# Kernel optimization log

Measured on AMD Instinct MI355X. Metric: run time of the kernel, lower is better.

The kernel has to match this reference:

```python
import jax, jax.numpy as jnp
import numpy as np
import math

D = 8192      # data_dim = num simplices
B = 8         # batch
E = 131072    # Laplacian nnz (avg degree 16)
HID = 256     # hidden_dim
TDIM = 128    # time_embed_dim


def setup_inputs() -> dict:
    key = jax.random.key(0)
    ks = jax.random.split(key, 16)

    def lin(k, i, o):
        return jax.random.normal(k, (i, o), jnp.float32) / np.sqrt(i).astype(np.float32)

    return {
        "x": jax.random.normal(ks[0], (B, D), jnp.float32),
        "t": jax.random.uniform(ks[1], (B,), jnp.float32),
        "ld_idx": jax.random.randint(ks[2], (2, E), 0, D),
        "ld_val": jax.random.normal(ks[3], (E,), jnp.float32) * 0.1,
        "lu_idx": jax.random.randint(ks[4], (2, E), 0, D),
        "lu_val": jax.random.normal(ks[5], (E,), jnp.float32) * 0.1,
        "W1": jax.random.normal(ks[6], (1, HID, 3), jnp.float32),        # SNN layer1 weight [in, out, 1+down+up]
        "W2": jax.random.normal(ks[7], (HID, 1, 3), jnp.float32) / np.sqrt(HID).astype(np.float32),
        "t_w1": lin(ks[8], TDIM, HID), "t_b1": jnp.zeros((HID,), jnp.float32),
        "t_w2": lin(ks[9], HID, HID), "t_b2": jnp.zeros((HID,), jnp.float32),
        "map_w": lin(ks[10], D, HID), "map_b": jnp.zeros((HID,), jnp.float32),
        "o_w1": lin(ks[11], HID, HID), "o_b1": jnp.zeros((HID,), jnp.float32),
        "o_w2": lin(ks[12], HID, D), "o_b2": jnp.zeros((D,), jnp.float32),
    }


def timestep_embedding(t, dim, max_period=10000):
    half = dim // 2  # dim=128 is even, no zero padding column
    freqs = jnp.exp(-math.log(max_period) * jnp.arange(half, dtype=t.dtype) / half)
    args = t[:, None] * freqs[None, :]
    return jnp.concatenate([jnp.cos(args), jnp.sin(args)], axis=-1)


def spmm(idx, val, x):
    # sparse [N,N] @ dense [N,C] via COO gather + segment-sum scatter
    return jax.ops.segment_sum(val[:, None] * x[idx[1]], idx[0], num_segments=x.shape[0])


def snn_layer(x, W, ld_idx, ld_val, lu_idx, lu_val):
    # conv_order_down = conv_order_up = 1 -> terms: [identity, L_down x, L_up x]
    terms = jnp.stack([x, spmm(ld_idx, ld_val, x), spmm(lu_idx, lu_val, x)], axis=2)  # [N, Cin, 3]
    return jnp.einsum('nik,iok->no', terms, W)


def reference(x, t, ld_idx, ld_val, lu_idx, lu_val, W1, W2,
              t_w1, t_b1, t_w2, t_b2, map_w, map_b, o_w1, o_b1, o_w2, o_b2):
    # time embedding MLP
    t_emb = timestep_embedding(t, TDIM)                    # [B, TDIM]
    t_out = jax.nn.silu(t_emb @ t_w1 + t_b1) @ t_w2 + t_b2  # [B, HID]

    # SNN (2 layers): layer1 update_func=None -> raw y; layer2 update_func='id' -> raw y
    def snn(xi):  # xi: [N]
        h = snn_layer(xi[:, None], W1, ld_idx, ld_val, lu_idx, lu_val)  # [N, HID]
        y = snn_layer(h, W2, ld_idx, ld_val, lu_idx, lu_val)            # [N, 1]
        return y[:, 0]

    x_out = jax.vmap(snn)(x)                               # [B, N]

    # ResNet_FC with 0 res blocks -> just the map Linear
    h = x_out @ map_w + map_b                              # [B, HID]

    out = jax.nn.silu((h + t_out) @ o_w1 + o_b1) @ o_w2 + o_b2  # [B, D]
    return out
```

## Files before the change

kernel.cpp:

```cpp
#include <hip/hip_runtime.h>
#include <math.h>

#define D 8192
#define B 8
#define E 131072
#define HID 256
#define TDIM 128

#define OFF_XT 0
#define OFF_DD 65536
#define OFF_UU 131072
#define OFF_Y  196608
#define OFF_G  262144
#define OFF_SC 264192

__global__ __launch_bounds__(1024) void k_front(
        const float* __restrict__ x, const float* __restrict__ t,
        const float* __restrict__ W1, const float* __restrict__ W2,
        const float* __restrict__ t_w1, const float* __restrict__ t_b1,
        const float* __restrict__ t_w2, const float* __restrict__ t_b2,
        const float* __restrict__ map_b, float* __restrict__ ws)
{
    const int blk = blockIdx.x, tid = threadIdx.x;
    if (blk < 64) {
        int idx = blk * 1024 + tid;
        ws[OFF_XT + idx] = x[(idx & 7) * D + (idx >> 3)];
        ws[OFF_DD + idx] = 0.f;
        ws[OFF_UU + idx] = 0.f;
        ws[OFF_Y  + idx] = 0.f;
        return;
    }
    if (blk < 72) {
        const int b = blk - 64;
        __shared__ float emb[TDIM];
        __shared__ float h1[HID];
        __shared__ float part[4][HID];
        float tb = t[b];
        if (tid < TDIM) {
            int j = tid & 63;
            float freq = expf(-0.14391156831212787f * (float)j);
            float a = tb * freq;
            emb[tid] = (tid < 64) ? cosf(a) : sinf(a);
        }
        __syncthreads();
        const int j = tid & 255, ic = tid >> 8;
        float z = 0.f;
        #pragma unroll 8
        for (int i = ic * 32; i < ic * 32 + 32; i++) z += emb[i] * t_w1[i * HID + j];
        part[ic][j] = z;
        __syncthreads();
        if (tid < HID) {
            float zz = t_b1[tid] + part[0][tid] + part[1][tid] + part[2][tid] + part[3][tid];
            h1[tid] = zz / (1.f + expf(-zz));
        }
        __syncthreads();
        float z2 = 0.f;
        #pragma unroll 8
        for (int i = ic * 64; i < ic * 64 + 64; i++) z2 += h1[i] * t_w2[i * HID + j];
        part[ic][j] = z2;
        __syncthreads();
        if (tid < HID) {
            float zz = t_b2[tid] + part[0][tid] + part[1][tid] + part[2][tid] + part[3][tid];
            (ws + OFF_G)[b * HID + tid] = map_b[tid] + zz;
        }
        return;
    }
    {
        int w = tid >> 6, lane = tid & 63;
        if (w < 9) {
            int jj = w / 3, k = w % 3;
            float acc = 0.f;
            #pragma unroll
            for (int q = 0; q < 4; q++) {
                int i = lane + 64 * q;
                acc += W1[i * 3 + k] * W2[i * 3 + jj];
            }
            #pragma unroll
            for (int off = 32; off > 0; off >>= 1) acc += __shfl_down(acc, off, 64);
            if (lane == 0) (ws + OFF_SC)[jj * 3 + k] = acc;
        }
    }
}

__global__ void k_scat1(const int* __restrict__ ldi, const float* __restrict__ ldv,
                        const int* __restrict__ lui, const float* __restrict__ luv,
                        float* __restrict__ ws)
{
    int gtid = blockIdx.x * 256 + threadIdx.x;
    int b = gtid & 7;
    int e = gtid >> 3;
    const int* idx; const float* val; float* dst;
    if (e < E) { idx = ldi; val = ldv; dst = ws + OFF_DD; }
    else       { e -= E; idx = lui; val = luv; dst = ws + OFF_UU; }
    int row = idx[e];
    int col = idx[E + e];
    float v = val[e];
    atomicAdd(&dst[row * 8 + b], v * ws[OFF_XT + col * 8 + b]);
}

__global__ void k_scat2(const int* __restrict__ ldi, const float* __restrict__ ldv,
                        const int* __restrict__ lui, const float* __restrict__ luv,
                        float* __restrict__ ws)
{
    int gtid = blockIdx.x * 256 + threadIdx.x;
    int b = gtid & 7;
    int e = gtid >> 3;
    const float* sc = ws + OFF_SC;
    const int* idx; const float* val; float c0, c1, c2;
    if (e < E) { idx = ldi; val = ldv; c0 = sc[3]; c1 = sc[4]; c2 = sc[5]; }
    else       { e -= E; idx = lui; val = luv; c0 = sc[6]; c1 = sc[7]; c2 = sc[8]; }
    int row = idx[e];
    int col = idx[E + e];
    float v = val[e];
    int ci = col * 8 + b;
    float h = c0 * ws[OFF_XT + ci] + c1 * ws[OFF_DD + ci] + c2 * ws[OFF_UU + ci];
    atomicAdd(&ws[OFF_Y + row * 8 + b], v * h);
}

__global__ void k_map(const float* __restrict__ map_w, float* __restrict__ ws)
{
    __shared__ float yf[32 * 8];
    int blk = blockIdx.x, tid = threadIdx.x;
    const float* sc = ws + OFF_SC;
    float* g = ws + OFF_G;
    int base = blk * 256;
    yf[tid] = sc[0] * ws[OFF_XT + base + tid] + sc[1] * ws[OFF_DD + base + tid]
            + sc[2] * ws[OFF_UU + base + tid] + ws[OFF_Y + base + tid];
    __syncthreads();
    float acc[8] = {0.f, 0.f, 0.f, 0.f, 0.f, 0.f, 0.f, 0.f};
    int nbase = blk * 32;
    #pragma unroll 4
    for (int r = 0; r < 32; r++) {
        float w = map_w[(nbase + r) * HID + tid];
        #pragma unroll
        for (int b = 0; b < 8; b++) acc[b] += yf[r * 8 + b] * w;
    }
    #pragma unroll
    for (int b = 0; b < 8; b++) atomicAdd(&g[b * HID + tid], acc[b]);
}

__global__ __launch_bounds__(1024) void k_mlpout(
        const float* __restrict__ o_w1, const float* __restrict__ o_b1,
        const float* __restrict__ o_w2, const float* __restrict__ o_b2,
        const float* __restrict__ ws, float* __restrict__ out)
{
    __shared__ float gs[B * HID];
    __shared__ float part[4][B * HID];
    __shared__ float ssl[B * HID];
    const int blk = blockIdx.x, tid = threadIdx.x;
    gs[tid] = ws[OFF_G + tid];
    gs[1024 + tid] = ws[OFF_G + 1024 + tid];
    __syncthreads();
    {
        int j = tid & 255, ic = tid >> 8;
        float z[8] = {0.f, 0.f, 0.f, 0.f, 0.f, 0.f, 0.f, 0.f};
        #pragma unroll 4
        for (int i = ic * 64; i < ic * 64 + 64; i++) {
            float w = o_w1[i * HID + j];
            #pragma unroll
            for (int b = 0; b < 8; b++) z[b] += gs[b * HID + i] * w;
        }
        #pragma unroll
        for (int b = 0; b < 8; b++) part[ic][b * HID + j] = z[b];
    }
    __syncthreads();
    #pragma unroll
    for (int it = 0; it < 2; it++) {
        int P = it * 1024 + tid;
        float zz = o_b1[P & 255] + part[0][P] + part[1][P] + part[2][P] + part[3][P];
        ssl[P] = zz / (1.f + expf(-zz));
    }
    __syncthreads();
    {
        int nl = tid & 255, ic = tid >> 8;
        int n = blk * 256 + nl;
        float acc[8] = {0.f, 0.f, 0.f, 0.f, 0.f, 0.f, 0.f, 0.f};
        #pragma unroll 4
        for (int j = ic * 64; j < ic * 64 + 64; j++) {
            float w = o_w2[j * D + n];
            #pragma unroll
            for (int b = 0; b < 8; b++) acc[b] += ssl[b * HID + j] * w;
        }
        #pragma unroll
        for (int b = 0; b < 8; b++) part[ic][b * HID + nl] = acc[b];
    }
    __syncthreads();
    #pragma unroll
    for (int it = 0; it < 2; it++) {
        int P = it * 1024 + tid;
        int b = P >> 8, nl = P & 255;
        int n = blk * 256 + nl;
        out[b * D + n] = o_b2[n] + part[0][P] + part[1][P] + part[2][P] + part[3][P];
    }
}

extern "C" void kernel_launch(void* const* d_in, const int* in_sizes, int n_in,
                              void* d_out, int out_size, void* d_ws, size_t ws_size,
                              hipStream_t stream)
{
    const float* x     = (const float*)d_in[0];
    const float* t     = (const float*)d_in[1];
    const int*   ldi   = (const int*)  d_in[2];
    const float* ldv   = (const float*)d_in[3];
    const int*   lui   = (const int*)  d_in[4];
    const float* luv   = (const float*)d_in[5];
    const float* W1    = (const float*)d_in[6];
    const float* W2    = (const float*)d_in[7];
    const float* t_w1  = (const float*)d_in[8];
    const float* t_b1  = (const float*)d_in[9];
    const float* t_w2  = (const float*)d_in[10];
    const float* t_b2  = (const float*)d_in[11];
    const float* map_w = (const float*)d_in[12];
    const float* map_b = (const float*)d_in[13];
    const float* o_w1  = (const float*)d_in[14];
    const float* o_b1  = (const float*)d_in[15];
    const float* o_w2  = (const float*)d_in[16];
    const float* o_b2  = (const float*)d_in[17];
    float* out = (float*)d_out;
    float* ws  = (float*)d_ws;

    k_front<<<73, 1024, 0, stream>>>(x, t, W1, W2, t_w1, t_b1, t_w2, t_b2, map_b, ws);
    k_scat1<<<2 * E * 8 / 256, 256, 0, stream>>>(ldi, ldv, lui, luv, ws);
    k_scat2<<<2 * E * 8 / 256, 256, 0, stream>>>(ldi, ldv, lui, luv, ws);
    k_map<<<256, 256, 0, stream>>>(map_w, ws);
    k_mlpout<<<32, 1024, 0, stream>>>(o_w1, o_b1, o_w2, o_b2, ws, out);
}
```

Before: 67.27 us.

## Replace atomic COO scatter SpMM with bucketed per-row gather SpMV

Builds per-row edge buckets (fixed capacity per row) once using integer atomic counters, then computes both Laplacian passes as row-wise gathers with one wavefront per row and shuffle reductions instead of float atomics per edge per batch. This removes the large volume of float atomicAdds and the zero-initialisation of accumulators, and folds the identity term into the second pass. It assumes no row exceeds the fixed bucket capacity, which holds for random degree-16 inputs but is not guaranteed generally, and the summation order becomes nondeterministic.

```diff
diff --git a/kernel.cpp b/kernel.cpp
--- a/kernel.cpp
+++ b/kernel.cpp
@@ -6,13 +6,17 @@
 #define E 131072
 #define HID 256
 #define TDIM 128
+#define MAXDEG 64
 
 #define OFF_XT 0
 #define OFF_DD 65536
 #define OFF_UU 131072
-#define OFF_Y  196608
-#define OFF_G  262144
-#define OFF_SC 264192
+#define OFF_Y0 196608
+#define OFF_Y1 262144
+#define OFF_G  327680
+#define OFF_SC 329728
+#define IOFF_CNT  329744
+#define IOFF_EDGE 346128
 
 __global__ __launch_bounds__(1024) void k_front(
         const float* __restrict__ x, const float* __restrict__ t,
@@ -25,9 +29,7 @@
     if (blk < 64) {
         int idx = blk * 1024 + tid;
         ws[OFF_XT + idx] = x[(idx & 7) * D + (idx >> 3)];
-        ws[OFF_DD + idx] = 0.f;
-        ws[OFF_UU + idx] = 0.f;
-        ws[OFF_Y  + idx] = 0.f;
+        if (idx < 16384) ((int*)ws)[IOFF_CNT + idx] = 0;
         return;
     }
     if (blk < 72) {
@@ -82,50 +84,83 @@
     }
 }
 
-__global__ void k_scat1(const int* __restrict__ ldi, const float* __restrict__ ldv,
-                        const int* __restrict__ lui, const float* __restrict__ luv,
-                        float* __restrict__ ws)
-{
-    int gtid = blockIdx.x * 256 + threadIdx.x;
-    int b = gtid & 7;
-    int e = gtid >> 3;
-    const int* idx; const float* val; float* dst;
-    if (e < E) { idx = ldi; val = ldv; dst = ws + OFF_DD; }
-    else       { e -= E; idx = lui; val = luv; dst = ws + OFF_UU; }
+__global__ void k_fill(const int* __restrict__ ldi, const float* __restrict__ ldv,
+                       const int* __restrict__ lui, const float* __restrict__ luv,
+                       float* __restrict__ ws)
+{
+    int t = blockIdx.x * 256 + threadIdx.x;
+    int m = t >> 17;
+    int e = t & (E - 1);
+    const int* idx = m ? lui : ldi;
+    const float* val = m ? luv : ldv;
     int row = idx[e];
     int col = idx[E + e];
     float v = val[e];
-    atomicAdd(&dst[row * 8 + b], v * ws[OFF_XT + col * 8 + b]);
-}
-
-__global__ void k_scat2(const int* __restrict__ ldi, const float* __restrict__ ldv,
-                        const int* __restrict__ lui, const float* __restrict__ luv,
-                        float* __restrict__ ws)
-{
-    int gtid = blockIdx.x * 256 + threadIdx.x;
-    int b = gtid & 7;
-    int e = gtid >> 3;
+    int bucket = m * D + row;
+    int slot = atomicAdd((int*)ws + IOFF_CNT + bucket, 1);
+    ((int2*)((int*)ws + IOFF_EDGE))[bucket * MAXDEG + slot] =
+        make_int2(col, __float_as_int(v));
+}
+
+__global__ void k_spmv1(float* __restrict__ ws)
+{
+    int wid = (blockIdx.x * 256 + threadIdx.x) >> 6;
+    int lane = threadIdx.x & 63;
+    int m = wid >> 13, r = wid & (D - 1);
+    int deg = ((const int*)ws)[IOFF_CNT + wid];
+    const int2* ep = (const int2*)((const int*)ws + IOFF_EDGE) + wid * MAXDEG;
+    int slot = lane >> 3, b = lane & 7;
+    float acc = 0.f;
+    for (int p = slot; p < deg; p += 8) {
+        int2 ed = ep[p];
+        acc += __int_as_float(ed.y) * ws[OFF_XT + ed.x * 8 + b];
+    }
+    acc += __shfl_xor(acc, 8, 64);
+    acc += __shfl_xor(acc, 16, 64);
+    acc += __shfl_xor(acc, 32, 64);
+    if (lane < 8) ws[(m ? OFF_UU : OFF_DD) + r * 8 + lane] = acc;
+}
+
+__global__ void k_spmv2(float* __restrict__ ws)
+{
+    int wid = (blockIdx.x * 256 + threadIdx.x) >> 6;
+    int lane = threadIdx.x & 63;
+    int m = wid >> 13, r = wid & (D - 1);
     const float* sc = ws + OFF_SC;
-    const int* idx; const float* val; float c0, c1, c2;
-    if (e < E) { idx = ldi; val = ldv; c0 = sc[3]; c1 = sc[4]; c2 = sc[5]; }
-    else       { e -= E; idx = lui; val = luv; c0 = sc[6]; c1 = sc[7]; c2 = sc[8]; }
-    int row = idx[e];
-    int col = idx[E + e];
-    float v = val[e];
-    int ci = col * 8 + b;
-    float h = c0 * ws[OFF_XT + ci] + c1 * ws[OFF_DD + ci] + c2 * ws[OFF_UU + ci];
-    atomicAdd(&ws[OFF_Y + row * 8 + b], v * h);
+    int deg = ((const int*)ws)[IOFF_CNT + wid];
+    const int2* ep = (const int2*)((const int*)ws + IOFF_EDGE) + wid * MAXDEG;
+    float c0, c1, c2;
+    if (m == 0) { c0 = sc[3]; c1 = sc[4]; c2 = sc[5]; }
+    else        { c0 = sc[6]; c1 = sc[7]; c2 = sc[8]; }
+    int slot = lane >> 3, b = lane & 7;
+    float acc = 0.f;
+    for (int p = slot; p < deg; p += 8) {
+        int2 ed = ep[p];
+        int ci = ed.x * 8 + b;
+        float h = c0 * ws[OFF_XT + ci] + c1 * ws[OFF_DD + ci] + c2 * ws[OFF_UU + ci];
+        acc += __int_as_float(ed.y) * h;
+    }
+    acc += __shfl_xor(acc, 8, 64);
+    acc += __shfl_xor(acc, 16, 64);
+    acc += __shfl_xor(acc, 32, 64);
+    if (lane < 8) {
+        int i = r * 8 + lane;
+        if (m == 0) {
+            acc += sc[0] * ws[OFF_XT + i] + sc[1] * ws[OFF_DD + i] + sc[2] * ws[OFF_UU + i];
+            ws[OFF_Y0 + i] = acc;
+        } else {
+            ws[OFF_Y1 + i] = acc;
+        }
+    }
 }
 
 __global__ void k_map(const float* __restrict__ map_w, float* __restrict__ ws)
 {
     __shared__ float yf[32 * 8];
     int blk = blockIdx.x, tid = threadIdx.x;
-    const float* sc = ws + OFF_SC;
     float* g = ws + OFF_G;
     int base = blk * 256;
-    yf[tid] = sc[0] * ws[OFF_XT + base + tid] + sc[1] * ws[OFF_DD + base + tid]
-            + sc[2] * ws[OFF_UU + base + tid] + ws[OFF_Y + base + tid];
+    yf[tid] = ws[OFF_Y0 + base + tid] + ws[OFF_Y1 + base + tid];
     __syncthreads();
     float acc[8] = {0.f, 0.f, 0.f, 0.f, 0.f, 0.f, 0.f, 0.f};
     int nbase = blk * 32;
@@ -220,8 +255,9 @@
     float* ws  = (float*)d_ws;
 
     k_front<<<73, 1024, 0, stream>>>(x, t, W1, W2, t_w1, t_b1, t_w2, t_b2, map_b, ws);
-    k_scat1<<<2 * E * 8 / 256, 256, 0, stream>>>(ldi, ldv, lui, luv, ws);
-    k_scat2<<<2 * E * 8 / 256, 256, 0, stream>>>(ldi, ldv, lui, luv, ws);
+    k_fill<<<2 * E / 256, 256, 0, stream>>>(ldi, ldv, lui, luv, ws);
+    k_spmv1<<<4096, 256, 0, stream>>>(ws);
+    k_spmv2<<<4096, 256, 0, stream>>>(ws);
     k_map<<<256, 256, 0, stream>>>(map_w, ws);
     k_mlpout<<<32, 1024, 0, stream>>>(o_w1, o_b1, o_w2, o_b2, ws, out);
 }
```

New measurement: 67.64 us. About the same (+0.6%).
